# Optimization experiments

Measured on AMD Instinct MI355X. Metric: run time of the kernel, lower is better.

The kernel has to match this reference:

```python
import jax, jax.numpy as jnp
import numpy as np

SEGMENT_LENGTHS = [1024, 4096]
DILATION_RATES = [1, 2]
HILBERT_CHUNK = 4096
B, N, H, D = 2, 4096, 16, 64


def _hilbert_mapping(n: int) -> np.ndarray:
    """Replicates _generate_hilbert_curve: gather indices for a length-n chunk."""
    if n <= 64:
        return np.arange(n, dtype=np.int64)
    size = 1
    while size * size < n:
        size *= 2

    def d2xy(nn, d):
        x = y = 0
        s = 1
        while s < nn:
            rx = 1 if (d // 2) & 1 else 0
            ry = 1 if (d ^ rx) & 1 else 0
            if ry == 0:
                if rx == 1:
                    x, y = nn - 1 - x, nn - 1 - y
                x, y = y, x
            x += s * rx
            y += s * ry
            d //= 4
            s *= 2
        return x, y

    mapping = np.zeros(n, dtype=np.int64)
    h2l = {}
    for i in range(min(n, size * size)):
        x, y = d2xy(size, i)
        li = y * size + x
        if li < n:
            h2l[i] = li
    hidx = 0
    for i in sorted(h2l):
        mapping[h2l[i]] = hidx
        hidx += 1
    return mapping


def _apply_hilbert(t: jnp.ndarray) -> jnp.ndarray:
    # t: [b, n, h, d]; reorder sequence within HILBERT_CHUNK-sized chunks.
    n = t.shape[1]
    chunks = []
    for start in range(0, n, HILBERT_CHUNK):
        end = min(start + HILBERT_CHUNK, n)
        m = jnp.asarray(_hilbert_mapping(end - start))
        chunks.append(t[:, start:end][:, m])
    return jnp.concatenate(chunks, axis=1) if len(chunks) > 1 else chunks[0]


def _dilation_indices(s: int, r: int, offset: int) -> np.ndarray:
    # Replicates _create_dilation_pattern
    idx = np.arange(offset, s, r, dtype=np.int64)
    expected = (s + r - 1 - offset) // r
    if idx.shape[0] > expected:
        idx = idx[:expected]
    elif idx.shape[0] < expected:
        pad = np.arange(expected - idx.shape[0], dtype=np.int64) % idx.shape[0]
        idx = np.concatenate([idx, idx[pad]])
    return idx


def _dilated_attention(q, k, v):
    # LongNet-style dilated attention: heads partitioned across groups;
    # each group attends within segments over dilated positions.
    b, n, h, d = q.shape
    G = len(SEGMENT_LENGTHS)
    hg = h // G
    scale = 1.0 / np.sqrt(d).astype(np.float32)
    out = jnp.zeros_like(q)
    for g, (s, r) in enumerate(zip(SEGMENT_LENGTHS, DILATION_RATES)):
        offset = g % r
        idx = jnp.asarray(_dilation_indices(s, r, offset))
        hs = slice(g * hg, (g + 1) * hg)
        # [b, n//s, s, hg, d] -> dilated [b, n//s, s/r, hg, d]
        qg = q[:, :, hs].reshape(b, n // s, s, hg, d)[:, :, idx]
        kg = k[:, :, hs].reshape(b, n // s, s, hg, d)[:, :, idx]
        vg = v[:, :, hs].reshape(b, n // s, s, hg, d)[:, :, idx]
        att = jnp.einsum('bgqhd,bgkhd->bghqk', qg, kg) * scale
        att = jax.nn.softmax(att, axis=-1)
        og = jnp.einsum('bghqk,bgkhd->bgqhd', att, vg)
        full = jnp.zeros((b, n // s, s, hg, d), q.dtype).at[:, :, idx].set(og)
        out = out.at[:, :, hs].set(full.reshape(b, n, hg, d))
    return out


def setup_inputs() -> dict:
    key = jax.random.key(0)
    kq, kk, kv = jax.random.split(key, 3)
    q = jax.random.normal(kq, (B, N, H, D), dtype=jnp.float32)
    k = jax.random.normal(kk, (B, N, H, D), dtype=jnp.float32)
    v = jax.random.normal(kv, (B, N, H, D), dtype=jnp.float32)
    return {'q': q, 'k': k, 'v': v}


def reference(q, k, v):
    k_h = _apply_hilbert(k)
    v_h = _apply_hilbert(v)
    return _dilated_attention(q, k_h, v_h)
```

## Files before the change

### kernel.cpp

```cpp
#include <hip/hip_runtime.h>
#include <hip/hip_bf16.h>

#define N_ 4096
#define H_ 16
#define D_ 64
#define G1ROWOFF 65536

typedef __attribute__((ext_vector_type(4))) float f32x4;
typedef __attribute__((ext_vector_type(8))) short bf16x8;

#define AS1 __attribute__((address_space(1)))
#define AS3 __attribute__((address_space(3)))

__device__ __forceinline__ unsigned int cvt2(float a, float b){
  __hip_bfloat16 ha = __float2bfloat16(a);
  __hip_bfloat16 hb = __float2bfloat16(b);
  unsigned short ua, ub;
  __builtin_memcpy(&ua, &ha, 2);
  __builtin_memcpy(&ub, &hb, 2);
  return (unsigned int)ua | ((unsigned int)ub << 16);
}

__global__ __launch_bounds__(1024) void hilbert_map_kernel(int* __restrict__ mapping){
  __shared__ int sm[4096];
  const int t = threadIdx.x;
#pragma unroll
  for(int jj=0;jj<4;jj++) mapping[t*4+jj] = 0;
  int li_a[4], val_a[4];
#pragma unroll
  for(int jj=0;jj<4;jj++){
    int i = t*4+jj;
    int x=0,y=0,d=i;
#pragma unroll
    for(int s=1;s<64;s<<=1){
      int rx=(d>>1)&1;
      int ry=(d^rx)&1;
      if(ry==0){
        if(rx==1){ x=63-x; y=63-y; }
        int tp=x; x=y; y=tp;
      }
      x+=s*rx; y+=s*ry;
      d>>=2;
    }
    int li=y*64+x;
    li_a[jj]=li;
    val_a[jj]=(li<4096)?1:0;
    sm[i]=val_a[jj];
  }
  __syncthreads();
  for(int off=1;off<4096;off<<=1){
    int v[4];
#pragma unroll
    for(int jj=0;jj<4;jj++){
      int i=t*4+jj;
      v[jj]=sm[i]+((i>=off)?sm[i-off]:0);
    }
    __syncthreads();
#pragma unroll
    for(int jj=0;jj<4;jj++) sm[t*4+jj]=v[jj];
    __syncthreads();
  }
#pragma unroll
  for(int jj=0;jj<4;jj++){
    if(val_a[jj]){
      int rank=sm[t*4+jj]-1;
      int li=li_a[jj];
      int wi=(li>=0)?li:(4096+li);
      if(wi>=0 && wi<4096) atomicMax(&mapping[wi], rank);
    }
  }
}

__global__ __launch_bounds__(256) void prep_kv_kernel(
    const float* __restrict__ K, const float* __restrict__ V,
    const int* __restrict__ hmap,
    unsigned short* __restrict__ Kb, unsigned short* __restrict__ Vt)
{
  __shared__ unsigned short Vlds[64*72];
  const int bid = blockIdx.x, tid = threadIdx.x;
  int b, h, dstRowBase, srcRow;
  const int r = tid>>2, part = tid&3;
  if (bid < 1024){
    int t64 = bid&63; h = (bid>>6)&7; b = bid>>9;
    dstRowBase = (b*8+h)*4096 + t64*64;
    srcRow = t64*64 + r;
  } else {
    int bid2 = bid-1024;
    int t64 = bid2&31; int h8 = (bid2>>5)&7; b = bid2>>8; h = 8+h8;
    dstRowBase = G1ROWOFF + (b*8+h8)*2048 + t64*64;
    srcRow = 1 + 2*(t64*64 + r);
  }
  const int src = hmap[srcRow];
  const size_t sb = (((size_t)(b*N_+src))*H_ + h)*D_ + part*16;
  {
    const float4* kp = (const float4*)(K + sb);
    float4 a=kp[0], c=kp[1], e=kp[2], g=kp[3];
    uint4 w0, w1;
    w0.x=cvt2(a.x,a.y); w0.y=cvt2(a.z,a.w); w0.z=cvt2(c.x,c.y); w0.w=cvt2(c.z,c.w);
    w1.x=cvt2(e.x,e.y); w1.y=cvt2(e.z,e.w); w1.z=cvt2(g.x,g.y); w1.w=cvt2(g.z,g.w);
    char* dst = (char*)Kb + ((size_t)(dstRowBase+r))*128;
    *(uint4*)(dst + ((2*part  )^(r&7))*16) = w0;
    *(uint4*)(dst + ((2*part+1)^(r&7))*16) = w1;
  }
  {
    const float4* vp = (const float4*)(V + sb);
    float4 a=vp[0], c=vp[1], e=vp[2], g=vp[3];
    uint4 w0, w1;
    w0.x=cvt2(a.x,a.y); w0.y=cvt2(a.z,a.w); w0.z=cvt2(c.x,c.y); w0.w=cvt2(c.z,c.w);
    w1.x=cvt2(e.x,e.y); w1.y=cvt2(e.z,e.w); w1.z=cvt2(g.x,g.y); w1.w=cvt2(g.z,g.w);
    uint4* dst=(uint4*)&Vlds[r*72 + part*16];
    dst[0]=w0; dst[1]=w1;
  }
  __syncthreads();
  {
    const int d = tid>>2, p2 = tid&3;
    unsigned int w[8];
#pragma unroll
    for(int jj=0;jj<8;jj++){
      unsigned int lo = Vlds[(p2*16 + 2*jj  )*72 + d];
      unsigned int hi = Vlds[(p2*16 + 2*jj+1)*72 + d];
      w[jj] = lo | (hi<<16);
    }
    uint4 w0, w1;
    w0.x=w[0]; w0.y=w[1]; w0.z=w[2]; w0.w=w[3];
    w1.x=w[4]; w1.y=w[5]; w1.z=w[6]; w1.w=w[7];
    char* dst = (char*)Vt + ((size_t)(dstRowBase+d))*128;
    *(uint4*)(dst + ((2*p2  )^(d&7))*16) = w0;
    *(uint4*)(dst + ((2*p2+1)^(d&7))*16) = w1;
  }
}

__global__ __launch_bounds__(256) void dilated_attn_kernel(
    const float* __restrict__ Q, const unsigned short* __restrict__ Kb,
    const unsigned short* __restrict__ Vt, float* __restrict__ Out)
{
  __shared__ __align__(16) char smem[49152];

  const int bid = blockIdx.x, tid = threadIdx.x;
  const int wave = tid>>6, lane = tid&63;
  const int lr = lane&15, lg = lane>>4;

  int b, outH, nt, qstep, qoff, qlocal0, rowBase;
  if (bid < 256){
    int H    = (bid&7) + 8*(bid>>7);
    int kblk = (bid>>3)&15;
    b = H>>3; outH = 8 + (H&7);
    nt = 32; qstep = 2; qoff = 1;
    qlocal0 = kblk*128;
    rowBase = G1ROWOFF + H*2048;
    int i = tid>>1, half = tid&1;
    int zpos = 2*(qlocal0 + i);
    float4 z = {0.f,0.f,0.f,0.f};
    float4* op = (float4*)(Out + (((size_t)(b*N_+zpos))*H_ + outH)*D_ + half*32);
#pragma unroll
    for(int j=0;j<8;j++) op[j]=z;
  } else {
    int p = bid - 256;
    int G    = (p&7) + 8*(p>>6);
    int kblk = (p>>3)&7;
    b = G>>5; int seg=(G>>3)&3; int h=G&7; outH=h;
    nt = 16; qstep = 1; qoff = 0;
    qlocal0 = seg*1024 + kblk*128;
    rowBase = (b*8+h)*4096 + seg*1024;
  }

  const float SCL = 0.125f * 1.4426950408889634f;
  bf16x8 qf[2][2];
#pragma unroll
  for(int qs=0;qs<2;qs++){
    int qpos = qoff + qstep*(qlocal0 + wave*32 + qs*16 + lr);
    const float* qp = Q + (((size_t)(b*N_+qpos))*H_ + outH)*D_;
#pragma unroll
    for(int dc=0;dc<2;dc++){
      float4 a = *(const float4*)(qp + dc*32 + lg*8);
      float4 c = *(const float4*)(qp + dc*32 + lg*8 + 4);
      union{ unsigned int u[4]; bf16x8 v; } pk;
      pk.u[0]=cvt2(a.x*SCL,a.y*SCL); pk.u[1]=cvt2(a.z*SCL,a.w*SCL);
      pk.u[2]=cvt2(c.x*SCL,c.y*SCL); pk.u[3]=cvt2(c.z*SCL,c.w*SCL);
      qf[qs][dc]=pk.v;
    }
  }

  f32x4 acc[2][4];
  f32x4 accl[2];
#pragma unroll
  for(int qs=0;qs<2;qs++){
#pragma unroll
    for(int dt=0;dt<4;dt++){ acc[qs][dt][0]=0.f; acc[qs][dt][1]=0.f; acc[qs][dt][2]=0.f; acc[qs][dt][3]=0.f; }
    accl[qs][0]=0.f; accl[qs][1]=0.f; accl[qs][2]=0.f; accl[qs][3]=0.f;
  }
  union{ unsigned int u[4]; bf16x8 v; } ONES;
  ONES.u[0]=0x3F803F80u; ONES.u[1]=0x3F803F80u; ONES.u[2]=0x3F803F80u; ONES.u[3]=0x3F803F80u;

  const int swz = lr&7;
  const int kA0 = lr*128 + ((  lg)^swz)*16;
  const int kA1 = lr*128 + ((4+lg)^swz)*16;
  int vA[2][2];
#pragma unroll
  for(int c=0;c<2;c++)
#pragma unroll
    for(int u=0;u<2;u++)
      vA[c][u] = 8192 + lr*128 + ((4*c+2*u+(lg>>1))^swz)*16 + (lg&1)*8;

  const char* gK = (const char*)Kb + (size_t)rowBase*128;
  const char* gV = (const char*)Vt + (size_t)rowBase*128;

  const char* gBase = (wave<2) ? gK : gV;
  const int sOff = ((wave<2) ? tid : (tid-128))*16;
  const int sHalf = (wave<2) ? 0 : 8192;
  auto stage = [&](char* buf, int t){
    const char* gsrc = gBase + (size_t)t*8192 + sOff;
    char* ldst = buf + sHalf + sOff;
#pragma unroll
    for(int i=0;i<4;i++){
      __builtin_amdgcn_global_load_lds((const AS1 void*)(gsrc + i*2048),
                                       (AS3 void*)(ldst + i*2048), 16, 0, 0);
    }
  };

  auto compute = [&](const char* sm){
    f32x4 s[2][4];
#pragma unroll
    for(int qs=0;qs<2;qs++)
#pragma unroll
      for(int kt=0;kt<4;kt++){ s[qs][kt][0]=0.f; s[qs][kt][1]=0.f; s[qs][kt][2]=0.f; s[qs][kt][3]=0.f; }
    __builtin_amdgcn_s_setprio(1);
#pragma unroll
    for(int kt=0;kt<4;kt++){
      bf16x8 k0 = *(const bf16x8*)(sm + kA0 + kt*2048);
      bf16x8 k1 = *(const bf16x8*)(sm + kA1 + kt*2048);
#pragma unroll
      for(int qs=0;qs<2;qs++){
        s[qs][kt] = __builtin_amdgcn_mfma_f32_16x16x32_bf16(k0, qf[qs][0], s[qs][kt],0,0,0);
        s[qs][kt] = __builtin_amdgcn_mfma_f32_16x16x32_bf16(k1, qf[qs][1], s[qs][kt],0,0,0);
      }
    }
    __builtin_amdgcn_s_setprio(0);
    unsigned int U[2][4][2];
#pragma unroll
    for(int qs=0;qs<2;qs++)
#pragma unroll
      for(int kt=0;kt<4;kt++){
        float p0 = __builtin_amdgcn_exp2f(s[qs][kt][0]);
        float p1 = __builtin_amdgcn_exp2f(s[qs][kt][1]);
        float p2 = __builtin_amdgcn_exp2f(s[qs][kt][2]);
        float p3 = __builtin_amdgcn_exp2f(s[qs][kt][3]);
        U[qs][kt][0] = cvt2(p0,p1);
        U[qs][kt][1] = cvt2(p2,p3);
      }
    __builtin_amdgcn_s_setprio(1);
#pragma unroll
    for(int c=0;c<2;c++){
      union{ unsigned int u[4]; bf16x8 v; } pf0, pf1;
      pf0.u[0]=U[0][2*c][0]; pf0.u[1]=U[0][2*c][1]; pf0.u[2]=U[0][2*c+1][0]; pf0.u[3]=U[0][2*c+1][1];
      pf1.u[0]=U[1][2*c][0]; pf1.u[1]=U[1][2*c][1]; pf1.u[2]=U[1][2*c+1][0]; pf1.u[3]=U[1][2*c+1][1];
#pragma unroll
      for(int dt=0;dt<4;dt++){
        uint2 lo = *(const uint2*)(sm + vA[c][0] + dt*2048);
        uint2 hi = *(const uint2*)(sm + vA[c][1] + dt*2048);
        union{ unsigned int u[4]; bf16x8 v; } vf;
        vf.u[0]=lo.x; vf.u[1]=lo.y; vf.u[2]=hi.x; vf.u[3]=hi.y;
        acc[0][dt] = __builtin_amdgcn_mfma_f32_16x16x32_bf16(pf0.v, vf.v, acc[0][dt],0,0,0);
        acc[1][dt] = __builtin_amdgcn_mfma_f32_16x16x32_bf16(pf1.v, vf.v, acc[1][dt],0,0,0);
      }
      accl[0] = __builtin_amdgcn_mfma_f32_16x16x32_bf16(pf0.v, ONES.v, accl[0],0,0,0);
      accl[1] = __builtin_amdgcn_mfma_f32_16x16x32_bf16(pf1.v, ONES.v, accl[1],0,0,0);
    }
    __builtin_amdgcn_s_setprio(0);
  };

  char* bA = smem;
  char* bB = smem + 16384;
  char* bC = smem + 32768;
  stage(bA, 0);
  stage(bB, 1);
  for(int t=0; t<nt-2; ++t){
    asm volatile("s_waitcnt vmcnt(4)" ::: "memory");
    __builtin_amdgcn_s_barrier();
    stage(bC, t+2);
    compute(bA);
    char* tmp=bA; bA=bB; bB=bC; bC=tmp;
  }
  asm volatile("s_waitcnt vmcnt(4)" ::: "memory");
  __builtin_amdgcn_s_barrier();
  compute(bA);
  asm volatile("s_waitcnt vmcnt(0)" ::: "memory");
  __builtin_amdgcn_s_barrier();
  compute(bB);

#pragma unroll
  for(int qs=0;qs<2;qs++){
#pragma unroll
    for(int r=0;r<4;r++){
      float inv = 1.0f/accl[qs][r];
      int qpos = qoff + qstep*(qlocal0 + wave*32 + qs*16 + lg*4 + r);
      float* op = Out + (((size_t)(b*N_+qpos))*H_ + outH)*D_ + lr;
#pragma unroll
      for(int dt=0;dt<4;dt++) op[dt*16] = acc[qs][dt][r]*inv;
    }
  }
}

extern "C" void kernel_launch(void* const* d_in, const int* in_sizes, int n_in,
                              void* d_out, int out_size, void* d_ws, size_t ws_size,
                              hipStream_t stream){
  const float* Q = (const float*)d_in[0];
  const float* K = (const float*)d_in[1];
  const float* V = (const float*)d_in[2];
  float* Out = (float*)d_out;

  int* hmap = (int*)d_ws;
  unsigned short* Kb = (unsigned short*)((char*)d_ws + 16384);
  unsigned short* Vt = (unsigned short*)((char*)d_ws + 16384 + 12582912);

  hipLaunchKernelGGL(hilbert_map_kernel, dim3(1), dim3(1024), 0, stream, hmap);
  hipLaunchKernelGGL(prep_kv_kernel, dim3(1536), dim3(256), 0, stream, K, V, hmap, Kb, Vt);
  hipLaunchKernelGGL(dilated_attn_kernel, dim3(768), dim3(256), 0, stream, Q, Kb, Vt, Out);
}
```

Measured before the change: 82.67 us.

## Merge group-0 query blocks into two-job workgroups and contiguous V fragment layout

Group-0 workgroups now process two query blocks of the same segment back to back in one continuous pipelined stream of 32 tiles, cutting the grid from 768 to 512 blocks so that all blocks carry equal work. The V transpose in the prep kernel is re-permuted so the PV MFMA operand is one 16-byte LDS read instead of two 8-byte reads. The first QK MFMA also takes a zero constant accumulator, which drops the explicit zeroing. K/V tiles are reloaded per job rather than reused, and the fixed tile count for the pipeline tail is hardcoded to 32.

```diff
diff --git a/kernel.cpp b/kernel.cpp
--- a/kernel.cpp
+++ b/kernel.cpp
@@ -19,6 +19,9 @@
   __builtin_memcpy(&ua, &ha, 2);
   __builtin_memcpy(&ub, &hb, 2);
   return (unsigned int)ua | ((unsigned int)ub << 16);
+}
+__device__ __forceinline__ unsigned int pku(unsigned int lo, unsigned int hi){
+  return lo | (hi << 16);
 }
 
 __global__ __launch_bounds__(1024) void hilbert_map_kernel(int* __restrict__ mapping){
@@ -114,19 +117,19 @@
   __syncthreads();
   {
     const int d = tid>>2, p2 = tid&3;
-    unsigned int w[8];
-#pragma unroll
-    for(int jj=0;jj<8;jj++){
-      unsigned int lo = Vlds[(p2*16 + 2*jj  )*72 + d];
-      unsigned int hi = Vlds[(p2*16 + 2*jj+1)*72 + d];
-      w[jj] = lo | (hi<<16);
-    }
-    uint4 w0, w1;
-    w0.x=w[0]; w0.y=w[1]; w0.z=w[2]; w0.w=w[3];
-    w1.x=w[4]; w1.y=w[5]; w1.z=w[6]; w1.w=w[7];
+    unsigned int w0[4], w1[4];
+#pragma unroll
+    for(int c=0;c<2;c++){
+      int kb = 32*c + 4*p2;
+      unsigned int* w = c ? w1 : w0;
+      w[0] = pku(Vlds[(kb+ 0)*72+d], Vlds[(kb+ 1)*72+d]);
+      w[1] = pku(Vlds[(kb+ 2)*72+d], Vlds[(kb+ 3)*72+d]);
+      w[2] = pku(Vlds[(kb+16)*72+d], Vlds[(kb+17)*72+d]);
+      w[3] = pku(Vlds[(kb+18)*72+d], Vlds[(kb+19)*72+d]);
+    }
     char* dst = (char*)Vt + ((size_t)(dstRowBase+d))*128;
-    *(uint4*)(dst + ((2*p2  )^(d&7))*16) = w0;
-    *(uint4*)(dst + ((2*p2+1)^(d&7))*16) = w1;
+    *(uint4*)(dst + ((p2  )^(d&7))*16) = *(uint4*)w0;
+    *(uint4*)(dst + ((p2+4)^(d&7))*16) = *(uint4*)w1;
   }
 }
 
@@ -140,77 +143,75 @@
   const int wave = tid>>6, lane = tid&63;
   const int lr = lane&15, lg = lane>>4;
 
-  int b, outH, nt, qstep, qoff, qlocal0, rowBase;
+  int b, outH, qstep, qoff, njobs, ntj;
+  int qloc[2];
+  size_t kb0, kb1;
   if (bid < 256){
-    int H    = (bid&7) + 8*(bid>>7);
-    int kblk = (bid>>3)&15;
+    int xcd = bid&7, idx = bid>>3;
+    int kblk = idx&15, Hp = idx>>4;
+    int H = xcd + 8*Hp;
     b = H>>3; outH = 8 + (H&7);
-    nt = 32; qstep = 2; qoff = 1;
-    qlocal0 = kblk*128;
-    rowBase = G1ROWOFF + H*2048;
+    qstep = 2; qoff = 1; njobs = 1; ntj = 32;
+    qloc[0] = kblk*128; qloc[1] = qloc[0];
+    size_t rowBase = (size_t)G1ROWOFF + (size_t)H*2048;
+    kb0 = rowBase*128; kb1 = kb0 + 16*8192;
     int i = tid>>1, half = tid&1;
-    int zpos = 2*(qlocal0 + i);
+    int zpos = 2*(qloc[0] + i);
     float4 z = {0.f,0.f,0.f,0.f};
     float4* op = (float4*)(Out + (((size_t)(b*N_+zpos))*H_ + outH)*D_ + half*32);
 #pragma unroll
     for(int j=0;j<8;j++) op[j]=z;
   } else {
     int p = bid - 256;
-    int G    = (p&7) + 8*(p>>6);
-    int kblk = (p>>3)&7;
+    int xcd = p&7, idx = p>>3;
+    int pair = idx&3, Gp = idx>>2;
+    int G = xcd + 8*Gp;
     b = G>>5; int seg=(G>>3)&3; int h=G&7; outH=h;
-    nt = 16; qstep = 1; qoff = 0;
-    qlocal0 = seg*1024 + kblk*128;
-    rowBase = (b*8+h)*4096 + seg*1024;
+    qstep = 1; qoff = 0; njobs = 2; ntj = 16;
+    qloc[0] = seg*1024 + pair*128;
+    qloc[1] = seg*1024 + (pair+4)*128;
+    size_t rowBase = ((size_t)(b*8+h))*4096 + (size_t)seg*1024;
+    kb0 = rowBase*128; kb1 = kb0;
   }
 
   const float SCL = 0.125f * 1.4426950408889634f;
   bf16x8 qf[2][2];
-#pragma unroll
-  for(int qs=0;qs<2;qs++){
-    int qpos = qoff + qstep*(qlocal0 + wave*32 + qs*16 + lr);
-    const float* qp = Q + (((size_t)(b*N_+qpos))*H_ + outH)*D_;
-#pragma unroll
-    for(int dc=0;dc<2;dc++){
-      float4 a = *(const float4*)(qp + dc*32 + lg*8);
-      float4 c = *(const float4*)(qp + dc*32 + lg*8 + 4);
-      union{ unsigned int u[4]; bf16x8 v; } pk;
-      pk.u[0]=cvt2(a.x*SCL,a.y*SCL); pk.u[1]=cvt2(a.z*SCL,a.w*SCL);
-      pk.u[2]=cvt2(c.x*SCL,c.y*SCL); pk.u[3]=cvt2(c.z*SCL,c.w*SCL);
-      qf[qs][dc]=pk.v;
-    }
-  }
-
   f32x4 acc[2][4];
   f32x4 accl[2];
-#pragma unroll
-  for(int qs=0;qs<2;qs++){
-#pragma unroll
-    for(int dt=0;dt<4;dt++){ acc[qs][dt][0]=0.f; acc[qs][dt][1]=0.f; acc[qs][dt][2]=0.f; acc[qs][dt][3]=0.f; }
-    accl[qs][0]=0.f; accl[qs][1]=0.f; accl[qs][2]=0.f; accl[qs][3]=0.f;
-  }
+  const f32x4 FZ = {0.f,0.f,0.f,0.f};
   union{ unsigned int u[4]; bf16x8 v; } ONES;
   ONES.u[0]=0x3F803F80u; ONES.u[1]=0x3F803F80u; ONES.u[2]=0x3F803F80u; ONES.u[3]=0x3F803F80u;
+
+  auto loadQ = [&](int ql0){
+#pragma unroll
+    for(int qs=0;qs<2;qs++){
+      int qpos = qoff + qstep*(ql0 + wave*32 + qs*16 + lr);
+      const float* qp = Q + (((size_t)(b*N_+qpos))*H_ + outH)*D_;
+#pragma unroll
+      for(int dc=0;dc<2;dc++){
+        float4 a = *(const float4*)(qp + dc*32 + lg*8);
+        float4 c = *(const float4*)(qp + dc*32 + lg*8 + 4);
+        union{ unsigned int u[4]; bf16x8 v; } pk;
+        pk.u[0]=cvt2(a.x*SCL,a.y*SCL); pk.u[1]=cvt2(a.z*SCL,a.w*SCL);
+        pk.u[2]=cvt2(c.x*SCL,c.y*SCL); pk.u[3]=cvt2(c.z*SCL,c.w*SCL);
+        qf[qs][dc]=pk.v;
+      }
+    }
+  };
 
   const int swz = lr&7;
   const int kA0 = lr*128 + ((  lg)^swz)*16;
   const int kA1 = lr*128 + ((4+lg)^swz)*16;
-  int vA[2][2];
-#pragma unroll
-  for(int c=0;c<2;c++)
-#pragma unroll
-    for(int u=0;u<2;u++)
-      vA[c][u] = 8192 + lr*128 + ((4*c+2*u+(lg>>1))^swz)*16 + (lg&1)*8;
-
-  const char* gK = (const char*)Kb + (size_t)rowBase*128;
-  const char* gV = (const char*)Vt + (size_t)rowBase*128;
-
-  const char* gBase = (wave<2) ? gK : gV;
-  const int sOff = ((wave<2) ? tid : (tid-128))*16;
+  const int vA0 = 8192 + lr*128 + ((  lg)^swz)*16;
+  const int vA1 = 8192 + lr*128 + ((4+lg)^swz)*16;
+
+  const char* gBase = (wave<2) ? (const char*)Kb : (const char*)Vt;
+  const int sOff = (tid&127)*16;
   const int sHalf = (wave<2) ? 0 : 8192;
-  auto stage = [&](char* buf, int t){
-    const char* gsrc = gBase + (size_t)t*8192 + sOff;
-    char* ldst = buf + sHalf + sOff;
+  auto stage = [&](int bufOff, int t){
+    size_t off = ((t>=16)? kb1 : kb0) + (size_t)(t&15)*8192 + sOff;
+    const char* gsrc = gBase + off;
+    char* ldst = smem + bufOff + sHalf + sOff;
 #pragma unroll
     for(int i=0;i<4;i++){
       __builtin_amdgcn_global_load_lds((const AS1 void*)(gsrc + i*2048),
@@ -218,12 +219,9 @@
     }
   };
 
-  auto compute = [&](const char* sm){
+  auto compute = [&](int bufOff){
+    const char* sm = smem + bufOff;
     f32x4 s[2][4];
-#pragma unroll
-    for(int qs=0;qs<2;qs++)
-#pragma unroll
-      for(int kt=0;kt<4;kt++){ s[qs][kt][0]=0.f; s[qs][kt][1]=0.f; s[qs][kt][2]=0.f; s[qs][kt][3]=0.f; }
     __builtin_amdgcn_s_setprio(1);
 #pragma unroll
     for(int kt=0;kt<4;kt++){
@@ -231,7 +229,7 @@
       bf16x8 k1 = *(const bf16x8*)(sm + kA1 + kt*2048);
 #pragma unroll
       for(int qs=0;qs<2;qs++){
-        s[qs][kt] = __builtin_amdgcn_mfma_f32_16x16x32_bf16(k0, qf[qs][0], s[qs][kt],0,0,0);
+        s[qs][kt] = __builtin_amdgcn_mfma_f32_16x16x32_bf16(k0, qf[qs][0], FZ, 0,0,0);
         s[qs][kt] = __builtin_amdgcn_mfma_f32_16x16x32_bf16(k1, qf[qs][1], s[qs][kt],0,0,0);
       }
     }
@@ -254,14 +252,12 @@
       union{ unsigned int u[4]; bf16x8 v; } pf0, pf1;
       pf0.u[0]=U[0][2*c][0]; pf0.u[1]=U[0][2*c][1]; pf0.u[2]=U[0][2*c+1][0]; pf0.u[3]=U[0][2*c+1][1];
       pf1.u[0]=U[1][2*c][0]; pf1.u[1]=U[1][2*c][1]; pf1.u[2]=U[1][2*c+1][0]; pf1.u[3]=U[1][2*c+1][1];
+      const int vAc = c ? vA1 : vA0;
 #pragma unroll
       for(int dt=0;dt<4;dt++){
-        uint2 lo = *(const uint2*)(sm + vA[c][0] + dt*2048);
-        uint2 hi = *(const uint2*)(sm + vA[c][1] + dt*2048);
-        union{ unsigned int u[4]; bf16x8 v; } vf;
-        vf.u[0]=lo.x; vf.u[1]=lo.y; vf.u[2]=hi.x; vf.u[3]=hi.y;
-        acc[0][dt] = __builtin_amdgcn_mfma_f32_16x16x32_bf16(pf0.v, vf.v, acc[0][dt],0,0,0);
-        acc[1][dt] = __builtin_amdgcn_mfma_f32_16x16x32_bf16(pf1.v, vf.v, acc[1][dt],0,0,0);
+        bf16x8 vf = *(const bf16x8*)(sm + vAc + dt*2048);
+        acc[0][dt] = __builtin_amdgcn_mfma_f32_16x16x32_bf16(pf0.v, vf, acc[0][dt],0,0,0);
+        acc[1][dt] = __builtin_amdgcn_mfma_f32_16x16x32_bf16(pf1.v, vf, acc[1][dt],0,0,0);
       }
       accl[0] = __builtin_amdgcn_mfma_f32_16x16x32_bf16(pf0.v, ONES.v, accl[0],0,0,0);
       accl[1] = __builtin_amdgcn_mfma_f32_16x16x32_bf16(pf1.v, ONES.v, accl[1],0,0,0);
@@ -269,35 +265,39 @@
     __builtin_amdgcn_s_setprio(0);
   };
 
-  char* bA = smem;
-  char* bB = smem + 16384;
-  char* bC = smem + 32768;
-  stage(bA, 0);
-  stage(bB, 1);
-  for(int t=0; t<nt-2; ++t){
-    asm volatile("s_waitcnt vmcnt(4)" ::: "memory");
-    __builtin_amdgcn_s_barrier();
-    stage(bC, t+2);
-    compute(bA);
-    char* tmp=bA; bA=bB; bB=bC; bC=tmp;
-  }
-  asm volatile("s_waitcnt vmcnt(4)" ::: "memory");
-  __builtin_amdgcn_s_barrier();
-  compute(bA);
-  asm volatile("s_waitcnt vmcnt(0)" ::: "memory");
-  __builtin_amdgcn_s_barrier();
-  compute(bB);
-
-#pragma unroll
-  for(int qs=0;qs<2;qs++){
-#pragma unroll
-    for(int r=0;r<4;r++){
-      float inv = 1.0f/accl[qs][r];
-      int qpos = qoff + qstep*(qlocal0 + wave*32 + qs*16 + lg*4 + r);
-      float* op = Out + (((size_t)(b*N_+qpos))*H_ + outH)*D_ + lr;
-#pragma unroll
-      for(int dt=0;dt<4;dt++) op[dt*16] = acc[qs][dt][r]*inv;
-    }
+  auto epilogue = [&](int ql0){
+#pragma unroll
+    for(int qs=0;qs<2;qs++)
+#pragma unroll
+      for(int r=0;r<4;r++){
+        float inv = 1.0f/accl[qs][r];
+        int qpos = qoff + qstep*(ql0 + wave*32 + qs*16 + lg*4 + r);
+        float* op = Out + (((size_t)(b*N_+qpos))*H_ + outH)*D_ + lr;
+#pragma unroll
+        for(int dt=0;dt<4;dt++) op[dt*16] = acc[qs][dt][r]*inv;
+      }
+  };
+
+  stage(0, 0);
+  stage(16384, 1);
+  int tglob = 0;
+  const int bOff[3] = {0, 16384, 32768};
+  for(int j=0; j<njobs; ++j){
+    loadQ(qloc[j]);
+#pragma unroll
+    for(int qs=0;qs<2;qs++){
+#pragma unroll
+      for(int dt=0;dt<4;dt++) acc[qs][dt] = FZ;
+      accl[qs] = FZ;
+    }
+    for(int tt=0; tt<ntj; ++tt, ++tglob){
+      if (tglob < 31) { asm volatile("s_waitcnt vmcnt(4)" ::: "memory"); }
+      else            { asm volatile("s_waitcnt vmcnt(0)" ::: "memory"); }
+      __builtin_amdgcn_s_barrier();
+      if (tglob < 30) stage(bOff[(tglob+2)%3], tglob+2);
+      compute(bOff[tglob%3]);
+    }
+    epilogue(qloc[j]);
   }
 }
 
@@ -315,5 +315,5 @@
 
   hipLaunchKernelGGL(hilbert_map_kernel, dim3(1), dim3(1024), 0, stream, hmap);
   hipLaunchKernelGGL(prep_kv_kernel, dim3(1536), dim3(256), 0, stream, K, V, hmap, Kb, Vt);
-  hipLaunchKernelGGL(dilated_attn_kernel, dim3(768), dim3(256), 0, stream, Q, Kb, Vt, Out);
-}
+  hipLaunchKernelGGL(dilated_attn_kernel, dim3(512), dim3(256), 0, stream, Q, Kb, Vt, Out);
+}
```

Result: faster. 76.51 us (-7.4%).
